# Kernel optimization log

Hardware: AMD Instinct MI355X
Metric: run time of the kernel (lower is better)

The kernel has to match this reference:

```python
import jax, jax.numpy as jnp
import numpy as np

EPS_BN = 1e-5
NEG_SLOPE = 0.2

def gat_layer(x, src, dst, N, W, a_src, a_dst, b, heads, ch, concat):
    # x: [N, Fin]; W: [Fin, heads*ch]; a_src/a_dst: [heads, ch]; b: [heads*ch] or [ch]
    xw = (x @ W).reshape(N, heads, ch)                      # [N,H,C]
    al_src = jnp.einsum('nhc,hc->nh', xw, a_src)            # [N,H]
    al_dst = jnp.einsum('nhc,hc->nh', xw, a_dst)
    e = jax.nn.leaky_relu(al_src[src] + al_dst[dst], NEG_SLOPE)  # [E,H]
    m = jax.ops.segment_max(e, dst, num_segments=N)         # segment softmax (stable)
    ee = jnp.exp(e - m[dst])
    s = jax.ops.segment_sum(ee, dst, num_segments=N)
    alpha = ee / (s[dst] + 1e-16)                            # [E,H]
    msg = xw[src] * alpha[:, :, None]                        # [E,H,C]
    out = jax.ops.segment_sum(msg, dst, num_segments=N)      # [N,H,C]
    if concat:
        return out.reshape(N, heads * ch) + b
    return out.mean(axis=1) + b

def setup_inputs():
    key = jax.random.key(0)
    ks = jax.random.split(key, 24)
    N, E, dim_in, dim_out = 20000, 320000, 256, 16
    x = jax.random.normal(ks[0], (N, dim_in), dtype=jnp.float32)
    edge_index = jax.random.randint(ks[1], (2, E), 0, N, dtype=jnp.int64)
    def glorot(k, shape):
        fan = shape[0] + shape[-1]
        return jax.random.uniform(k, shape, jnp.float32, -1.0, 1.0) * np.sqrt(6.0 / fan)
    return {
        'x': x, 'edge_index': edge_index,
        'bn_gamma': jnp.ones((dim_in,), jnp.float32),
        'bn_beta': jnp.zeros((dim_in,), jnp.float32),
        'W1': glorot(ks[2], (dim_in, 16 * 64)),
        'a1_src': glorot(ks[3], (16, 64)), 'a1_dst': glorot(ks[4], (16, 64)),
        'b1': jnp.zeros((16 * 64,), jnp.float32),
        'p1': jnp.float32(0.25),
        'W2': glorot(ks[5], (dim_in + 16 * 64, 8 * 8)),
        'a2_src': glorot(ks[6], (8, 8)), 'a2_dst': glorot(ks[7], (8, 8)),
        'b2': jnp.zeros((8 * 8,), jnp.float32),
        'p2': jnp.float32(0.25),
        'W3': glorot(ks[8], (8 * 8, 8 * dim_out)),
        'a3_src': glorot(ks[9], (8, dim_out)), 'a3_dst': glorot(ks[10], (8, dim_out)),
        'b3': jnp.zeros((dim_out,), jnp.float32),
    }

def reference(x, edge_index, bn_gamma, bn_beta, W1, a1_src, a1_dst, b1, p1,
              W2, a2_src, a2_dst, b2, p2, W3, a3_src, a3_dst, b3):
    N = x.shape[0]
    # PyG GATConv default add_self_loops=True
    loops = jnp.arange(N, dtype=edge_index.dtype)
    src = jnp.concatenate([edge_index[0], loops])
    dst = jnp.concatenate([edge_index[1], loops])
    # BatchNorm1d (training-mode batch stats)
    mu = x.mean(axis=0)
    var = x.var(axis=0)
    x_in = (x - mu) * jax.lax.rsqrt(var + EPS_BN) * bn_gamma + bn_beta
    h = gat_layer(x_in, src, dst, N, W1, a1_src, a1_dst, b1, 16, 64, True)
    h = jnp.where(h >= 0, h, p1 * h)  # PReLU
    h = gat_layer(jnp.concatenate([x_in, h], axis=1), src, dst, N, W2, a2_src, a2_dst, b2, 8, 8, True)
    h = jnp.where(h >= 0, h, p2 * h)
    h = gat_layer(h, src, dst, N, W3, a3_src, a3_dst, b3, 8, b3.shape[0], False)
    return jax.nn.log_softmax(h, axis=1)
```

## Files before the change

### kernel.cpp

```cpp
#include <hip/hip_runtime.h>
#include <math.h>

typedef unsigned int u32;
typedef unsigned short u16;
typedef u32 u32x4 __attribute__((ext_vector_type(4)));
typedef float f32x4 __attribute__((ext_vector_type(4)));

__device__ __forceinline__ u16 f2bf(float f) {
  u32 u = __builtin_bit_cast(u32, f);
  return (u16)((u + 0x7FFFu + ((u >> 16) & 1u)) >> 16);
}
__device__ __forceinline__ float bf2f(u32 lo16) {
  return __builtin_bit_cast(float, lo16 << 16);
}
__device__ __forceinline__ void mfma16(f32x4& c, const u32x4& a, const u32x4& b) {
  asm volatile("v_mfma_f32_16x16x32_bf16 %0, %1, %2, %0" : "+v"(c) : "v"(a), "v"(b));
}
__device__ __forceinline__ float lrelu(float e) { return fmaxf(e, 0.2f * e); }

__global__ void bn_stats_kernel(const float* __restrict__ x, float* __restrict__ musum,
                                float* __restrict__ sqsum, int N, int F) {
  int t = threadIdx.x;
  float s = 0.f, s2 = 0.f;
  for (int r = blockIdx.x; r < N; r += gridDim.x) {
    float v = x[(size_t)r * F + t];
    s += v;
    s2 += v * v;
  }
  atomicAdd(&musum[t], s);
  atomicAdd(&sqsum[t], s2);
}

__global__ void bn_finalize_kernel(const float* __restrict__ musum, const float* __restrict__ sqsum,
                                   const float* __restrict__ gamma, const float* __restrict__ beta,
                                   float* __restrict__ scale, float* __restrict__ shift, int N) {
  int t = threadIdx.x;
  float m = musum[t] / (float)N;
  float v = sqsum[t] / (float)N - m * m;
  float sc = gamma[t] * rsqrtf(v + 1e-5f);
  scale[t] = sc;
  shift[t] = beta[t] - m * sc;
}

__global__ void bn_apply_bf16_kernel(const float* __restrict__ x, const float* __restrict__ scale,
                                     const float* __restrict__ shift, u16* __restrict__ xin,
                                     int total, int Fmask) {
  int i = blockIdx.x * blockDim.x + threadIdx.x;
  if (i < total) {
    int c = i & Fmask;
    xin[i] = f2bf(x[i] * scale[c] + shift[c]);
  }
}

__global__ void csr_count_kernel(const int* __restrict__ ei, int E, int N, int* __restrict__ cnt) {
  int e = blockIdx.x * blockDim.x + threadIdx.x;
  int ET = E + N;
  if (e < ET) {
    int d = (e < E) ? ei[E + e] : (e - E);
    atomicAdd(&cnt[d], 1);
  }
}

__global__ __launch_bounds__(1024) void csr_scan_kernel(const int* __restrict__ cnt,
                                                        int* __restrict__ row_ptr,
                                                        int* __restrict__ cursor, int N) {
  __shared__ int part[1024];
  int t = threadIdx.x;
  int chunk = (N + 1023) / 1024;
  int lo = t * chunk;
  int hi = min(lo + chunk, N);
  int s = 0;
  for (int i = lo; i < hi; i++) s += cnt[i];
  part[t] = s;
  __syncthreads();
  for (int off = 1; off < 1024; off <<= 1) {
    int v = (t >= off) ? part[t - off] : 0;
    __syncthreads();
    part[t] += v;
    __syncthreads();
  }
  int run = (t == 0) ? 0 : part[t - 1];
  for (int i = lo; i < hi; i++) {
    row_ptr[i] = run;
    cursor[i] = run;
    run += cnt[i];
  }
  if (t == 1023) row_ptr[N] = part[1023];
}

__global__ void csr_fill_kernel(const int* __restrict__ ei, int E, int N,
                                int* __restrict__ cursor, int* __restrict__ csr_src) {
  int e = blockIdx.x * blockDim.x + threadIdx.x;
  int ET = E + N;
  if (e < ET) {
    int s, d;
    if (e < E) { s = ei[e]; d = ei[E + e]; }
    else       { s = e - E; d = s; }
    int pos = atomicAdd(&cursor[d], 1);
    csr_src[pos] = s;
  }
}

__global__ __launch_bounds__(1024) void perm_build_kernel(const int* __restrict__ row_ptr,
                                                          int* __restrict__ perm, int N) {
  __shared__ int bins[256];
  __shared__ int base[256];
  int t = threadIdx.x;
  if (t < 256) bins[t] = 0;
  __syncthreads();
  for (int i = t; i < N; i += 1024) {
    int d = min(row_ptr[i + 1] - row_ptr[i], 255);
    atomicAdd(&bins[d], 1);
  }
  __syncthreads();
  for (int off = 1; off < 256; off <<= 1) {
    int u = (t < 256 && t >= off) ? bins[t - off] : 0;
    __syncthreads();
    if (t < 256) bins[t] += u;
    __syncthreads();
  }
  if (t < 256) base[t] = (t == 0) ? 0 : bins[t - 1];
  __syncthreads();
  if (t < 256) bins[t] = base[t];
  __syncthreads();
  for (int i = t; i < N; i += 1024) {
    int d = min(row_ptr[i + 1] - row_ptr[i], 255);
    int pos = atomicAdd(&bins[d], 1);
    perm[pos] = i;
  }
}

__global__ void wt_build_all(const float* __restrict__ W1, const float* __restrict__ W2,
                             const float* __restrict__ W3, u16* __restrict__ Wt1,
                             u16* __restrict__ Wt2, u16* __restrict__ Wt3) {
  const int S1 = 1024 * 256, S2 = 64 * 1280, S3 = 128 * 64;
  const int P1 = 96 * 256, P2 = 32 * 1280, P3 = 32 * 64;
  int idx = blockIdx.x * blockDim.x + threadIdx.x;
  if (idx < S1) {
    int n = idx / 256, k = idx % 256;
    Wt1[idx] = f2bf(W1[(size_t)k * 1024 + n]);
  } else if (idx < S1 + S2) {
    int i = idx - S1;
    int n = i / 1280, k = i % 1280;
    Wt2[i] = f2bf(W2[(size_t)k * 64 + n]);
  } else if (idx < S1 + S2 + S3) {
    int i = idx - S1 - S2;
    int n = i / 64, k = i % 64;
    Wt3[i] = f2bf(W3[(size_t)k * 128 + n]);
  } else if (idx < S1 + S2 + S3 + P1) {
    Wt1[S1 + (idx - S1 - S2 - S3)] = 0;
  } else if (idx < S1 + S2 + S3 + P1 + P2) {
    Wt2[S2 + (idx - S1 - S2 - S3 - P1)] = 0;
  } else if (idx < S1 + S2 + S3 + P1 + P2 + P3) {
    Wt3[S3 + (idx - S1 - S2 - S3 - P1 - P2)] = 0;
  }
}

__global__ void alfold_build(const float* __restrict__ W1, const float* __restrict__ a1s,
                             const float* __restrict__ a1d, const float* __restrict__ W2,
                             const float* __restrict__ a2s, const float* __restrict__ a2d,
                             const float* __restrict__ W3, const float* __restrict__ a3s,
                             const float* __restrict__ a3d, u16* __restrict__ Wt1,
                             u16* __restrict__ Wt2, u16* __restrict__ Wt3) {
  const int T1 = 32 * 256, T2 = 16 * 1280, T3 = 16 * 64;
  int idx = blockIdx.x * blockDim.x + threadIdx.x;
  if (idx < T1) {
    int jj = idx / 256, k = idx % 256, h = jj >> 1;
    const float* av = (jj & 1) ? a1d : a1s;
    float s = 0.f;
    for (int c = 0; c < 64; c++) s += W1[(size_t)k * 1024 + h * 64 + c] * av[h * 64 + c];
    Wt1[(size_t)(1024 + jj) * 256 + k] = f2bf(s);
  } else if (idx < T1 + T2) {
    int i = idx - T1;
    int jj = i / 1280, k = i % 1280, h = jj >> 1;
    const float* av = (jj & 1) ? a2d : a2s;
    float s = 0.f;
    for (int c = 0; c < 8; c++) s += W2[(size_t)k * 64 + h * 8 + c] * av[h * 8 + c];
    Wt2[(size_t)(64 + jj) * 1280 + k] = f2bf(s);
  } else if (idx < T1 + T2 + T3) {
    int i = idx - T1 - T2;
    int jj = i / 64, k = i % 64, h = jj >> 1;
    const float* av = (jj & 1) ? a3d : a3s;
    float s = 0.f;
    for (int c = 0; c < 16; c++) s += W3[(size_t)k * 128 + h * 16 + c] * av[h * 16 + c];
    Wt3[(size_t)(128 + jj) * 64 + k] = f2bf(s);
  }
}

template <int BM, int BN, int FM, int FN>
__global__ __launch_bounds__(256) void mfma_gemm_al(
    const u16* __restrict__ A1, const u16* __restrict__ A2, int K1, int K,
    const u16* __restrict__ Wt, u16* __restrict__ Ch, int NcH,
    float* __restrict__ als, float* __restrict__ ald, int ALN, int ALP, int M) {
  constexpr int BK = 32;
  constexpr int ACH = (BM * BK) / 8;
  constexpr int BCH = (BN * BK) / 8;
  static_assert(BM == 2 * FM * 16 && BN == 2 * FN * 16, "wave grid 2x2");
  __shared__ u16 As[2][BM * BK];
  __shared__ u16 Bs[2][BN * BK];
  int t = threadIdx.x;
  int m0 = blockIdx.x * BM, n0 = blockIdx.y * BN;
  int r = t & 15;
  int g = (t >> 4) & 3;
  int wid = t >> 6;
  int wm0 = (wid >> 1) * (FM * 16);
  int wn0 = (wid & 1) * (FN * 16);
  int K8 = K >> 3;
  int K2 = K - K1;

  auto stage = [&](int buf, int k0) {
    const u16* Aseg;
    int sA, kl;
    if (k0 < K1) { Aseg = A1; sA = K1; kl = k0; }
    else         { Aseg = A2; sA = K2; kl = k0 - K1; }
#pragma unroll
    for (int i = 0; i < (ACH + 255) / 256; i++) {
      int c = i * 256 + t;
      if (ACH % 256 == 0 || c < ACH) {
        int m = c >> 2, kb = c & 3;
        __builtin_amdgcn_global_load_lds(
            (const __attribute__((address_space(1))) void*)(Aseg + (size_t)(m0 + m) * sA + kl + kb * 8),
            (__attribute__((address_space(3))) void*)(&As[buf][c * 8]), 16, 0, 0);
      }
    }
#pragma unroll
    for (int i = 0; i < (BCH + 255) / 256; i++) {
      int c = i * 256 + t;
      if (BCH % 256 == 0 || c < BCH) {
        int nn = c >> 2, kb = c & 3;
        __builtin_amdgcn_global_load_lds(
            (const __attribute__((address_space(1))) void*)(Wt + ((size_t)(n0 + nn) * K8 + (k0 >> 3) + kb) * 8),
            (__attribute__((address_space(3))) void*)(&Bs[buf][c * 8]), 16, 0, 0);
      }
    }
  };

  f32x4 acc[FM][FN] = {};
  asm volatile("s_nop 7\n\ts_nop 7" :::);

  stage(0, 0);
  __syncthreads();
  int nt = K / BK;
  for (int ts = 0; ts < nt; ts++) {
    if (ts + 1 < nt) stage((ts + 1) & 1, (ts + 1) * BK);
    int cur = ts & 1;
    u32x4 af[FM], bfr[FN];
#pragma unroll
    for (int fi = 0; fi < FM; fi++)
      af[fi] = *(const u32x4*)(&As[cur][((wm0 + fi * 16 + r) * 4 + g) * 8]);
#pragma unroll
    for (int fj = 0; fj < FN; fj++)
      bfr[fj] = *(const u32x4*)(&Bs[cur][((wn0 + fj * 16 + r) * 4 + g) * 8]);
#pragma unroll
    for (int fi = 0; fi < FM; fi++)
#pragma unroll
      for (int fj = 0; fj < FN; fj++) mfma16(acc[fi][fj], af[fi], bfr[fj]);
    __syncthreads();
  }
  asm volatile("s_nop 7\n\ts_nop 7" :::);

#pragma unroll
  for (int fi = 0; fi < FM; fi++) {
#pragma unroll
    for (int fj = 0; fj < FN; fj++) {
#pragma unroll
      for (int v = 0; v < 4; v++) {
        int m = m0 + wm0 + fi * 16 + g * 4 + v;
        int nn = n0 + wn0 + fj * 16 + r;
        if (m < M) {
          float val = acc[fi][fj][v];
          if (nn < NcH) {
            Ch[(size_t)m * NcH + nn] = f2bf(val);
          } else {
            int j = nn - NcH;
            if (j < ALN) ((j & 1) ? ald : als)[(size_t)(j >> 1) * ALP + m] = val;
          }
        }
      }
    }
  }
}

__global__ __launch_bounds__(256) void gat_agg1_gs(
    const u16* __restrict__ xwh, const float* __restrict__ alsrc,
    const float* __restrict__ aldst, const int* __restrict__ row_ptr,
    const int* __restrict__ csr_src, const int* __restrict__ perm,
    const float* __restrict__ bias, const float* __restrict__ slope_p,
    u16* __restrict__ out, int N, int ALP, int NBH) {
  constexpr int U = 4;
  int b = blockIdx.x;
  int xcd = b & 7, seq = b >> 3;
  int phase = seq / NBH, nb = seq - phase * NBH;
  int h = xcd + (phase << 3);
  int lane = threadIdx.x & 63;
  int g = lane >> 3, l8 = lane & 7;
  int ti = nb * 32 + (threadIdx.x >> 6) * 8 + g;
  int n = perm[min(ti, N - 1)];
  const float* alh = alsrc + (size_t)h * ALP;
  float ad = aldst[(size_t)h * ALP + n];
  int start = row_ptr[n];
  int end = row_ptr[n + 1];
  int deg = (ti < N) ? end - start : 0;
  int endm1 = end - 1;

  float m = -1e30f, s = 0.f;
  float acc[8] = {};
  const u16* base = xwh + (size_t)h * 64 + (size_t)l8 * 8;

  auto fma8 = [&](const u32x4& v, float w) {
#pragma unroll
    for (int i = 0; i < 4; i++) {
      u32 u = v[i];
      acc[2 * i] = fmaf(w, bf2f(u & 0xffffu), acc[2 * i]);
      acc[2 * i + 1] = fmaf(w, bf2f(u >> 16), acc[2 * i + 1]);
    }
  };

  int c[U];
#pragma unroll
  for (int i = 0; i < U; i++) c[i] = csr_src[min(start + i, endm1)];
  int j = 0;
  for (; j + U <= deg; j += U) {
    u32x4 v[U];
    float e[U];
#pragma unroll
    for (int i = 0; i < U; i++) v[i] = *(const u32x4*)(base + (size_t)c[i] * 1024);
#pragma unroll
    for (int i = 0; i < U; i++) e[i] = lrelu(alh[c[i]] + ad);
#pragma unroll
    for (int i = 0; i < U; i++) c[i] = csr_src[min(start + j + U + i, endm1)];
    float mn = fmaxf(fmaxf(e[0], e[1]), fmaxf(e[2], e[3]));
    if (mn > m) {
      float sc = __expf(m - mn);
      s *= sc;
#pragma unroll
      for (int k = 0; k < 8; k++) acc[k] *= sc;
      m = mn;
    }
#pragma unroll
    for (int i = 0; i < U; i++) {
      float w = __expf(e[i] - m);
      s += w;
      fma8(v[i], w);
    }
  }
  for (int i = 0; j < deg; j++, i++) {
    u32x4 v = *(const u32x4*)(base + (size_t)c[i] * 1024);
    float e = lrelu(alh[c[i]] + ad);
    if (e > m) {
      float sc = __expf(m - e);
      s *= sc;
#pragma unroll
      for (int k = 0; k < 8; k++) acc[k] *= sc;
      m = e;
    }
    float w = __expf(e - m);
    s += w;
    fma8(v, w);
  }
  float rr = 1.f / (s + 1e-16f);

  if (ti < N) {
    float p = slope_p[0];
    u32 ow[4];
#pragma unroll
    for (int i = 0; i < 4; i++) {
      int cc = h * 64 + l8 * 8 + 2 * i;
      float v0 = acc[2 * i] * rr + bias[cc];
      float v1 = acc[2 * i + 1] * rr + bias[cc + 1];
      v0 = (v0 >= 0.f) ? v0 : p * v0;
      v1 = (v1 >= 0.f) ? v1 : p * v1;
      ow[i] = (u32)f2bf(v0) | ((u32)f2bf(v1) << 16);
    }
    *(u32x4*)(out + (size_t)n * 1024 + h * 64 + l8 * 8) = *(u32x4*)ow;
  }
}

__global__ __launch_bounds__(256) void gat_agg2_gs(
    const u16* __restrict__ xwh, const float* __restrict__ alsrc,
    const float* __restrict__ aldst, const int* __restrict__ row_ptr,
    const int* __restrict__ csr_src, const int* __restrict__ perm,
    const float* __restrict__ bias, const float* __restrict__ slope_p,
    u16* __restrict__ out, int N, int ALP) {
  constexpr int U = 4;
  int lane = threadIdx.x & 63;
  int g = lane >> 3, l8 = lane & 7;
  int ti = blockIdx.x * 32 + (threadIdx.x >> 6) * 8 + g;
  int n = perm[min(ti, N - 1)];
  const float* alh = alsrc + (size_t)l8 * ALP;
  float ad = aldst[(size_t)l8 * ALP + n];
  int start = row_ptr[n];
  int end = row_ptr[n + 1];
  int deg = (ti < N) ? end - start : 0;
  int endm1 = end - 1;

  float m = -1e30f, s = 0.f;
  float acc[8] = {};
  const u16* base = xwh + (size_t)l8 * 8;

  auto fma8 = [&](const u32x4& v, float w) {
#pragma unroll
    for (int i = 0; i < 4; i++) {
      u32 u = v[i];
      acc[2 * i] = fmaf(w, bf2f(u & 0xffffu), acc[2 * i]);
      acc[2 * i + 1] = fmaf(w, bf2f(u >> 16), acc[2 * i + 1]);
    }
  };

  int c[U];
#pragma unroll
  for (int i = 0; i < U; i++) c[i] = csr_src[min(start + i, endm1)];
  int j = 0;
  for (; j + U <= deg; j += U) {
    u32x4 v[U];
    float e[U];
#pragma unroll
    for (int i = 0; i < U; i++) v[i] = *(const u32x4*)(base + (size_t)c[i] * 64);
#pragma unroll
    for (int i = 0; i < U; i++) e[i] = lrelu(alh[c[i]] + ad);
#pragma unroll
    for (int i = 0; i < U; i++) c[i] = csr_src[min(start + j + U + i, endm1)];
    float mn = fmaxf(fmaxf(e[0], e[1]), fmaxf(e[2], e[3]));
    if (mn > m) {
      float sc = __expf(m - mn);
      s *= sc;
#pragma unroll
      for (int k = 0; k < 8; k++) acc[k] *= sc;
      m = mn;
    }
#pragma unroll
    for (int i = 0; i < U; i++) {
      float w = __expf(e[i] - m);
      s += w;
      fma8(v[i], w);
    }
  }
  for (int i = 0; j < deg; j++, i++) {
    u32x4 v = *(const u32x4*)(base + (size_t)c[i] * 64);
    float e = lrelu(alh[c[i]] + ad);
    if (e > m) {
      float sc = __expf(m - e);
      s *= sc;
#pragma unroll
      for (int k = 0; k < 8; k++) acc[k] *= sc;
      m = e;
    }
    float w = __expf(e - m);
    s += w;
    fma8(v, w);
  }
  float rr = 1.f / (s + 1e-16f);

  if (ti < N) {
    float p = slope_p[0];
    u32 ow[4];
#pragma unroll
    for (int i = 0; i < 4; i++) {
      int cc = l8 * 8 + 2 * i;
      float v0 = acc[2 * i] * rr + bias[cc];
      float v1 = acc[2 * i + 1] * rr + bias[cc + 1];
      v0 = (v0 >= 0.f) ? v0 : p * v0;
      v1 = (v1 >= 0.f) ? v1 : p * v1;
      ow[i] = (u32)f2bf(v0) | ((u32)f2bf(v1) << 16);
    }
    *(u32x4*)(out + (size_t)n * 64 + l8 * 8) = *(u32x4*)ow;
  }
}

__global__ __launch_bounds__(256) void gat_agg3_gs(
    const u16* __restrict__ xwh, const float* __restrict__ alsrc,
    const float* __restrict__ aldst, const int* __restrict__ row_ptr,
    const int* __restrict__ csr_src, const int* __restrict__ perm,
    const float* __restrict__ bias, float* __restrict__ out, int N, int ALP) {
  constexpr int U = 4;
  int lane = threadIdx.x & 63;
  int g = lane >> 4, l16 = lane & 15;
  int head = l16 >> 1;
  int ti = blockIdx.x * 16 + (threadIdx.x >> 6) * 4 + g;
  int n = perm[min(ti, N - 1)];
  const float* alh = alsrc + (size_t)head * ALP;
  float ad = aldst[(size_t)head * ALP + n];
  int start = row_ptr[n];
  int end = row_ptr[n + 1];
  int deg = (ti < N) ? end - start : 0;
  int endm1 = end - 1;

  float m = -1e30f, s = 0.f;
  float acc[8] = {};
  const u16* base = xwh + (size_t)l16 * 8;

  auto fma8 = [&](const u32x4& v, float w) {
#pragma unroll
    for (int i = 0; i < 4; i++) {
      u32 u = v[i];
      acc[2 * i] = fmaf(w, bf2f(u & 0xffffu), acc[2 * i]);
      acc[2 * i + 1] = fmaf(w, bf2f(u >> 16), acc[2 * i + 1]);
    }
  };

  int c[U];
#pragma unroll
  for (int i = 0; i < U; i++) c[i] = csr_src[min(start + i, endm1)];
  int j = 0;
  for (; j + U <= deg; j += U) {
    u32x4 v[U];
    float e[U];
#pragma unroll
    for (int i = 0; i < U; i++) v[i] = *(const u32x4*)(base + (size_t)c[i] * 128);
#pragma unroll
    for (int i = 0; i < U; i++) e[i] = lrelu(alh[c[i]] + ad);
#pragma unroll
    for (int i = 0; i < U; i++) c[i] = csr_src[min(start + j + U + i, endm1)];
    float mn = fmaxf(fmaxf(e[0], e[1]), fmaxf(e[2], e[3]));
    if (mn > m) {
      float sc = __expf(m - mn);
      s *= sc;
#pragma unroll
      for (int k = 0; k < 8; k++) acc[k] *= sc;
      m = mn;
    }
#pragma unroll
    for (int i = 0; i < U; i++) {
      float w = __expf(e[i] - m);
      s += w;
      fma8(v[i], w);
    }
  }
  for (int i = 0; j < deg; j++, i++) {
    u32x4 v = *(const u32x4*)(base + (size_t)c[i] * 128);
    float e = lrelu(alh[c[i]] + ad);
    if (e > m) {
      float sc = __expf(m - e);
      s *= sc;
#pragma unroll
      for (int k = 0; k < 8; k++) acc[k] *= sc;
      m = e;
    }
    float w = __expf(e - m);
    s += w;
    fma8(v, w);
  }
  float rr = 1.f / (s + 1e-16f);
#pragma unroll
  for (int k = 0; k < 8; k++) acc[k] *= rr;

#pragma unroll
  for (int st = 2; st <= 8; st <<= 1)
#pragma unroll
    for (int k = 0; k < 8; k++) acc[k] += __shfl_xor(acc[k], st);

  int half = l16 & 1;
  float v8[8];
  float mx = -1e30f;
#pragma unroll
  for (int k = 0; k < 8; k++) {
    v8[k] = acc[k] * 0.125f + bias[half * 8 + k];
    mx = fmaxf(mx, v8[k]);
  }
  mx = fmaxf(mx, __shfl_xor(mx, 1));
  float se = 0.f;
#pragma unroll
  for (int k = 0; k < 8; k++) se += __expf(v8[k] - mx);
  se += __shfl_xor(se, 1);
  float lse = mx + logf(se);
  if (ti < N && l16 < 2) {
    float4 o0 = make_float4(v8[0] - lse, v8[1] - lse, v8[2] - lse, v8[3] - lse);
    float4 o1 = make_float4(v8[4] - lse, v8[5] - lse, v8[6] - lse, v8[7] - lse);
    float* op = out + (size_t)n * 16 + half * 8;
    *(float4*)op = o0;
    *(float4*)(op + 4) = o1;
  }
}

extern "C" void kernel_launch(void* const* d_in, const int* in_sizes, int n_in,
                              void* d_out, int out_size, void* d_ws, size_t ws_size,
                              hipStream_t stream) {
  const float* x        = (const float*)d_in[0];
  const int*   ei       = (const int*)d_in[1];
  const float* bn_gamma = (const float*)d_in[2];
  const float* bn_beta  = (const float*)d_in[3];
  const float* W1       = (const float*)d_in[4];
  const float* a1s      = (const float*)d_in[5];
  const float* a1d      = (const float*)d_in[6];
  const float* b1       = (const float*)d_in[7];
  const float* p1       = (const float*)d_in[8];
  const float* W2       = (const float*)d_in[9];
  const float* a2s      = (const float*)d_in[10];
  const float* a2d      = (const float*)d_in[11];
  const float* b2       = (const float*)d_in[12];
  const float* p2       = (const float*)d_in[13];
  const float* W3       = (const float*)d_in[14];
  const float* a3s      = (const float*)d_in[15];
  const float* a3d      = (const float*)d_in[16];
  const float* b3       = (const float*)d_in[17];
  float* out = (float*)d_out;

  const int F  = in_sizes[2];
  const int N  = in_sizes[0] / F;
  const int E  = in_sizes[1] / 2;
  const int ET = E + N;
  const int MP = ((N + 127) / 128) * 128;

  size_t off = 0;
  auto alloc = [&](size_t bytes) -> char* {
    char* r = (char*)d_ws + off;
    off += (bytes + 255) & ~(size_t)255;
    return r;
  };
  float* musum   = (float*)alloc(F * 4);
  float* sqsum   = (float*)alloc(F * 4);
  float* scale   = (float*)alloc(F * 4);
  float* shift   = (float*)alloc(F * 4);
  int*   row_ptr = (int*)alloc((size_t)(N + 1) * 4);
  int*   cursor  = (int*)alloc((size_t)N * 4);
  int*   csr_src = (int*)alloc((size_t)ET * 4);
  int*   perm    = (int*)alloc((size_t)N * 4);
  float* al_s    = (float*)alloc((size_t)16 * MP * 4);
  float* al_d    = (float*)alloc((size_t)16 * MP * 4);
  u16*   Wt1     = (u16*)alloc((size_t)1152 * 256 * 2);
  u16*   Wt2     = (u16*)alloc((size_t)96 * 1280 * 2);
  u16*   Wt3     = (u16*)alloc((size_t)160 * 64 * 2);
  u16*   x_in_h  = (u16*)alloc((size_t)MP * 256 * 2);
  u16*   xw1h    = (u16*)alloc((size_t)MP * 1024 * 2);
  u16*   h1      = (u16*)alloc((size_t)MP * 1024 * 2);
  u16*   xw2h    = (u16*)alloc((size_t)MP * 64 * 2);
  u16*   h2h     = (u16*)alloc((size_t)MP * 64 * 2);
  u16*   xw3h    = (u16*)alloc((size_t)MP * 128 * 2);

  hipMemsetAsync(musum, 0, (size_t)2 * F * 4, stream);
  bn_stats_kernel<<<256, 256, 0, stream>>>(x, musum, sqsum, N, F);
  bn_finalize_kernel<<<1, F, 0, stream>>>(musum, sqsum, bn_gamma, bn_beta, scale, shift, N);
  int totalXF = N * F;
  bn_apply_bf16_kernel<<<(totalXF + 255) / 256, 256, 0, stream>>>(x, scale, shift, x_in_h,
                                                                  totalXF, F - 1);

  hipMemsetAsync(cursor, 0, (size_t)N * 4, stream);
  csr_count_kernel<<<(ET + 255) / 256, 256, 0, stream>>>(ei, E, N, cursor);
  csr_scan_kernel<<<1, 1024, 0, stream>>>(cursor, row_ptr, cursor, N);
  csr_fill_kernel<<<(ET + 255) / 256, 256, 0, stream>>>(ei, E, N, cursor, csr_src);

  perm_build_kernel<<<1, 1024, 0, stream>>>(row_ptr, perm, N);

  {
    int total = 1024 * 256 + 64 * 1280 + 128 * 64 + 96 * 256 + 32 * 1280 + 32 * 64;
    wt_build_all<<<(total + 255) / 256, 256, 0, stream>>>(W1, W2, W3, Wt1, Wt2, Wt3);
    int tot2 = 32 * 256 + 16 * 1280 + 16 * 64;
    alfold_build<<<(tot2 + 255) / 256, 256, 0, stream>>>(W1, a1s, a1d, W2, a2s, a2d, W3, a3s, a3d,
                                                         Wt1, Wt2, Wt3);
  }

  {
    dim3 grid(MP / 128, 9);
    mfma_gemm_al<128, 128, 4, 4><<<grid, 256, 0, stream>>>(
        x_in_h, x_in_h, 256, 256, Wt1, xw1h, 1024, al_s, al_d, 32, MP, N);
    int NBH = (N + 31) / 32;
    gat_agg1_gs<<<8 * NBH * 2, 256, 0, stream>>>(xw1h, al_s, al_d, row_ptr, csr_src, perm, b1, p1,
                                                 h1, N, MP, NBH);
  }

  {
    dim3 grid((N + 63) / 64, 1);
    mfma_gemm_al<64, 96, 2, 3><<<grid, 256, 0, stream>>>(
        x_in_h, h1, 256, 1280, Wt2, xw2h, 64, al_s, al_d, 16, MP, N);
    gat_agg2_gs<<<(N + 31) / 32, 256, 0, stream>>>(xw2h, al_s, al_d, row_ptr, csr_src, perm, b2,
                                                   p2, h2h, N, MP);
  }

  {
    dim3 grid((N + 63) / 64, 1);
    mfma_gemm_al<64, 160, 2, 5><<<grid, 256, 0, stream>>>(
        h2h, h2h, 64, 64, Wt3, xw3h, 128, al_s, al_d, 16, MP, N);
    gat_agg3_gs<<<(N + 15) / 16, 256, 0, stream>>>(xw3h, al_s, al_d, row_ptr, csr_src, perm, b3,
                                                   out, N, MP);
  }
}
```

Before: 316.3 us.

## Fuse setup kernels to cut launches and raise layer-1 aggregation unroll

Merges BN finalize into the BN apply kernel, merges perm building into the CSR scan, and merges the weight transpose with the attention-fold build. It also folds the cursor memset into the stats memset. Together these remove several kernel launches and a memset from the fixed per-call overhead. The layer-1 aggregation unroll goes from 4 to 6 edges per iteration, which adds register pressure in exchange for more loads in flight. The zero-padding ranges were narrowed so they no longer overwrite the alfold rows in the same launch.

```diff
diff --git a/kernel.cpp b/kernel.cpp
--- a/kernel.cpp
+++ b/kernel.cpp
@@ -31,24 +31,19 @@
   atomicAdd(&sqsum[t], s2);
 }
 
-__global__ void bn_finalize_kernel(const float* __restrict__ musum, const float* __restrict__ sqsum,
-                                   const float* __restrict__ gamma, const float* __restrict__ beta,
-                                   float* __restrict__ scale, float* __restrict__ shift, int N) {
+__global__ void bn_apply_bf16_kernel(const float* __restrict__ x, const float* __restrict__ musum,
+                                     const float* __restrict__ sqsum,
+                                     const float* __restrict__ gamma,
+                                     const float* __restrict__ beta, u16* __restrict__ xin,
+                                     int N, float invN) {
   int t = threadIdx.x;
-  float m = musum[t] / (float)N;
-  float v = sqsum[t] / (float)N - m * m;
-  float sc = gamma[t] * rsqrtf(v + 1e-5f);
-  scale[t] = sc;
-  shift[t] = beta[t] - m * sc;
-}
-
-__global__ void bn_apply_bf16_kernel(const float* __restrict__ x, const float* __restrict__ scale,
-                                     const float* __restrict__ shift, u16* __restrict__ xin,
-                                     int total, int Fmask) {
-  int i = blockIdx.x * blockDim.x + threadIdx.x;
-  if (i < total) {
-    int c = i & Fmask;
-    xin[i] = f2bf(x[i] * scale[c] + shift[c]);
+  float mu = musum[t] * invN;
+  float var = sqsum[t] * invN - mu * mu;
+  float sc = gamma[t] * rsqrtf(var + 1e-5f);
+  float sh = beta[t] - mu * sc;
+  for (int r = blockIdx.x; r < N; r += gridDim.x) {
+    size_t idx = (size_t)r * 256 + t;
+    xin[idx] = f2bf(x[idx] * sc + sh);
   }
 }
 
@@ -61,16 +56,24 @@
   }
 }
 
-__global__ __launch_bounds__(1024) void csr_scan_kernel(const int* __restrict__ cnt,
-                                                        int* __restrict__ row_ptr,
-                                                        int* __restrict__ cursor, int N) {
+__global__ __launch_bounds__(1024) void csr_scan_perm_kernel(int* __restrict__ cnt,
+                                                             int* __restrict__ row_ptr,
+                                                             int* __restrict__ perm, int N) {
   __shared__ int part[1024];
+  __shared__ int bins[256];
+  __shared__ int bs[256];
   int t = threadIdx.x;
   int chunk = (N + 1023) / 1024;
-  int lo = t * chunk;
+  int lo = min(t * chunk, N);
   int hi = min(lo + chunk, N);
+  if (t < 256) bins[t] = 0;
+  __syncthreads();
   int s = 0;
-  for (int i = lo; i < hi; i++) s += cnt[i];
+  for (int i = lo; i < hi; i++) {
+    int d = cnt[i];
+    s += d;
+    atomicAdd(&bins[min(d, 255)], 1);
+  }
   part[t] = s;
   __syncthreads();
   for (int off = 1; off < 1024; off <<= 1) {
@@ -79,11 +82,28 @@
     part[t] += v;
     __syncthreads();
   }
+  if (t < 256) bs[t] = bins[t];
+  __syncthreads();
+  for (int off = 1; off < 256; off <<= 1) {
+    int v = (t < 256 && t >= off) ? bs[t - off] : 0;
+    __syncthreads();
+    if (t < 256) bs[t] += v;
+    __syncthreads();
+  }
+  if (t < 256) bins[t] = (t == 0) ? 0 : bs[t - 1];
+  __syncthreads();
+  for (int i = lo; i < hi; i++) {
+    int d = min(cnt[i], 255);
+    int pos = atomicAdd(&bins[d], 1);
+    perm[pos] = i;
+  }
+  __syncthreads();
   int run = (t == 0) ? 0 : part[t - 1];
   for (int i = lo; i < hi; i++) {
+    int d = cnt[i];
     row_ptr[i] = run;
-    cursor[i] = run;
-    run += cnt[i];
+    cnt[i] = run;
+    run += d;
   }
   if (t == 1023) row_ptr[N] = part[1023];
 }
@@ -101,90 +121,67 @@
   }
 }
 
-__global__ __launch_bounds__(1024) void perm_build_kernel(const int* __restrict__ row_ptr,
-                                                          int* __restrict__ perm, int N) {
-  __shared__ int bins[256];
-  __shared__ int base[256];
-  int t = threadIdx.x;
-  if (t < 256) bins[t] = 0;
-  __syncthreads();
-  for (int i = t; i < N; i += 1024) {
-    int d = min(row_ptr[i + 1] - row_ptr[i], 255);
-    atomicAdd(&bins[d], 1);
-  }
-  __syncthreads();
-  for (int off = 1; off < 256; off <<= 1) {
-    int u = (t < 256 && t >= off) ? bins[t - off] : 0;
-    __syncthreads();
-    if (t < 256) bins[t] += u;
-    __syncthreads();
-  }
-  if (t < 256) base[t] = (t == 0) ? 0 : bins[t - 1];
-  __syncthreads();
-  if (t < 256) bins[t] = base[t];
-  __syncthreads();
-  for (int i = t; i < N; i += 1024) {
-    int d = min(row_ptr[i + 1] - row_ptr[i], 255);
-    int pos = atomicAdd(&bins[d], 1);
-    perm[pos] = i;
-  }
-}
-
-__global__ void wt_build_all(const float* __restrict__ W1, const float* __restrict__ W2,
-                             const float* __restrict__ W3, u16* __restrict__ Wt1,
-                             u16* __restrict__ Wt2, u16* __restrict__ Wt3) {
+__global__ void wt_alfold_build(const float* __restrict__ W1, const float* __restrict__ a1s,
+                                const float* __restrict__ a1d, const float* __restrict__ W2,
+                                const float* __restrict__ a2s, const float* __restrict__ a2d,
+                                const float* __restrict__ W3, const float* __restrict__ a3s,
+                                const float* __restrict__ a3d, u16* __restrict__ Wt1,
+                                u16* __restrict__ Wt2, u16* __restrict__ Wt3) {
   const int S1 = 1024 * 256, S2 = 64 * 1280, S3 = 128 * 64;
-  const int P1 = 96 * 256, P2 = 32 * 1280, P3 = 32 * 64;
+  const int A1 = 32 * 256, A2 = 16 * 1280, A3 = 16 * 64;
+  const int Z1 = 96 * 256, Z2 = 16 * 1280, Z3 = 16 * 64;
   int idx = blockIdx.x * blockDim.x + threadIdx.x;
-  if (idx < S1) {
-    int n = idx / 256, k = idx % 256;
-    Wt1[idx] = f2bf(W1[(size_t)k * 1024 + n]);
-  } else if (idx < S1 + S2) {
-    int i = idx - S1;
-    int n = i / 1280, k = i % 1280;
-    Wt2[i] = f2bf(W2[(size_t)k * 64 + n]);
-  } else if (idx < S1 + S2 + S3) {
-    int i = idx - S1 - S2;
-    int n = i / 64, k = i % 64;
-    Wt3[i] = f2bf(W3[(size_t)k * 128 + n]);
-  } else if (idx < S1 + S2 + S3 + P1) {
-    Wt1[S1 + (idx - S1 - S2 - S3)] = 0;
-  } else if (idx < S1 + S2 + S3 + P1 + P2) {
-    Wt2[S2 + (idx - S1 - S2 - S3 - P1)] = 0;
-  } else if (idx < S1 + S2 + S3 + P1 + P2 + P3) {
-    Wt3[S3 + (idx - S1 - S2 - S3 - P1 - P2)] = 0;
-  }
-}
-
-__global__ void alfold_build(const float* __restrict__ W1, const float* __restrict__ a1s,
-                             const float* __restrict__ a1d, const float* __restrict__ W2,
-                             const float* __restrict__ a2s, const float* __restrict__ a2d,
-                             const float* __restrict__ W3, const float* __restrict__ a3s,
-                             const float* __restrict__ a3d, u16* __restrict__ Wt1,
-                             u16* __restrict__ Wt2, u16* __restrict__ Wt3) {
-  const int T1 = 32 * 256, T2 = 16 * 1280, T3 = 16 * 64;
-  int idx = blockIdx.x * blockDim.x + threadIdx.x;
-  if (idx < T1) {
-    int jj = idx / 256, k = idx % 256, h = jj >> 1;
+  int o = idx;
+  if (o < S1) {
+    int n = o / 256, k = o % 256;
+    Wt1[o] = f2bf(W1[(size_t)k * 1024 + n]);
+    return;
+  }
+  o -= S1;
+  if (o < S2) {
+    int n = o / 1280, k = o % 1280;
+    Wt2[o] = f2bf(W2[(size_t)k * 64 + n]);
+    return;
+  }
+  o -= S2;
+  if (o < S3) {
+    int n = o / 64, k = o % 64;
+    Wt3[o] = f2bf(W3[(size_t)k * 128 + n]);
+    return;
+  }
+  o -= S3;
+  if (o < A1) {
+    int jj = o / 256, k = o % 256, h = jj >> 1;
     const float* av = (jj & 1) ? a1d : a1s;
     float s = 0.f;
     for (int c = 0; c < 64; c++) s += W1[(size_t)k * 1024 + h * 64 + c] * av[h * 64 + c];
     Wt1[(size_t)(1024 + jj) * 256 + k] = f2bf(s);
-  } else if (idx < T1 + T2) {
-    int i = idx - T1;
-    int jj = i / 1280, k = i % 1280, h = jj >> 1;
+    return;
+  }
+  o -= A1;
+  if (o < A2) {
+    int jj = o / 1280, k = o % 1280, h = jj >> 1;
     const float* av = (jj & 1) ? a2d : a2s;
     float s = 0.f;
     for (int c = 0; c < 8; c++) s += W2[(size_t)k * 64 + h * 8 + c] * av[h * 8 + c];
     Wt2[(size_t)(64 + jj) * 1280 + k] = f2bf(s);
-  } else if (idx < T1 + T2 + T3) {
-    int i = idx - T1 - T2;
-    int jj = i / 64, k = i % 64, h = jj >> 1;
+    return;
+  }
+  o -= A2;
+  if (o < A3) {
+    int jj = o / 64, k = o % 64, h = jj >> 1;
     const float* av = (jj & 1) ? a3d : a3s;
     float s = 0.f;
     for (int c = 0; c < 16; c++) s += W3[(size_t)k * 128 + h * 16 + c] * av[h * 16 + c];
     Wt3[(size_t)(128 + jj) * 64 + k] = f2bf(s);
-  }
+    return;
+  }
+  o -= A3;
+  if (o < Z1) { Wt1[1056 * 256 + o] = 0; return; }
+  o -= Z1;
+  if (o < Z2) { Wt2[80 * 1280 + o] = 0; return; }
+  o -= Z2;
+  if (o < Z3) { Wt3[144 * 64 + o] = 0; return; }
 }
 
 template <int BM, int BN, int FM, int FN>
@@ -287,7 +284,7 @@
     const int* __restrict__ csr_src, const int* __restrict__ perm,
     const float* __restrict__ bias, const float* __restrict__ slope_p,
     u16* __restrict__ out, int N, int ALP, int NBH) {
-  constexpr int U = 4;
+  constexpr int U = 6;
   int b = blockIdx.x;
   int xcd = b & 7, seq = b >> 3;
   int phase = seq / NBH, nb = seq - phase * NBH;
@@ -329,7 +326,7 @@
     for (int i = 0; i < U; i++) e[i] = lrelu(alh[c[i]] + ad);
 #pragma unroll
     for (int i = 0; i < U; i++) c[i] = csr_src[min(start + j + U + i, endm1)];
-    float mn = fmaxf(fmaxf(e[0], e[1]), fmaxf(e[2], e[3]));
+    float mn = fmaxf(fmaxf(fmaxf(e[0], e[1]), fmaxf(e[2], e[3])), fmaxf(e[4], e[5]));
     if (mn > m) {
       float sc = __expf(m - mn);
       s *= sc;
@@ -609,10 +606,8 @@
   };
   float* musum   = (float*)alloc(F * 4);
   float* sqsum   = (float*)alloc(F * 4);
-  float* scale   = (float*)alloc(F * 4);
-  float* shift   = (float*)alloc(F * 4);
+  int*   cursor  = (int*)alloc((size_t)N * 4);
   int*   row_ptr = (int*)alloc((size_t)(N + 1) * 4);
-  int*   cursor  = (int*)alloc((size_t)N * 4);
   int*   csr_src = (int*)alloc((size_t)ET * 4);
   int*   perm    = (int*)alloc((size_t)N * 4);
   float* al_s    = (float*)alloc((size_t)16 * MP * 4);
@@ -627,26 +622,22 @@
   u16*   h2h     = (u16*)alloc((size_t)MP * 64 * 2);
   u16*   xw3h    = (u16*)alloc((size_t)MP * 128 * 2);
 
-  hipMemsetAsync(musum, 0, (size_t)2 * F * 4, stream);
+  hipMemsetAsync(musum, 0, (size_t)2 * F * 4 + (size_t)N * 4, stream);
+
   bn_stats_kernel<<<256, 256, 0, stream>>>(x, musum, sqsum, N, F);
-  bn_finalize_kernel<<<1, F, 0, stream>>>(musum, sqsum, bn_gamma, bn_beta, scale, shift, N);
-  int totalXF = N * F;
-  bn_apply_bf16_kernel<<<(totalXF + 255) / 256, 256, 0, stream>>>(x, scale, shift, x_in_h,
-                                                                  totalXF, F - 1);
-
-  hipMemsetAsync(cursor, 0, (size_t)N * 4, stream);
+  bn_apply_bf16_kernel<<<1024, 256, 0, stream>>>(x, musum, sqsum, bn_gamma, bn_beta, x_in_h, N,
+                                                 1.0f / (float)N);
+
   csr_count_kernel<<<(ET + 255) / 256, 256, 0, stream>>>(ei, E, N, cursor);
-  csr_scan_kernel<<<1, 1024, 0, stream>>>(cursor, row_ptr, cursor, N);
+  csr_scan_perm_kernel<<<1, 1024, 0, stream>>>(cursor, row_ptr, perm, N);
   csr_fill_kernel<<<(ET + 255) / 256, 256, 0, stream>>>(ei, E, N, cursor, csr_src);
 
-  perm_build_kernel<<<1, 1024, 0, stream>>>(row_ptr, perm, N);
-
   {
-    int total = 1024 * 256 + 64 * 1280 + 128 * 64 + 96 * 256 + 32 * 1280 + 32 * 64;
-    wt_build_all<<<(total + 255) / 256, 256, 0, stream>>>(W1, W2, W3, Wt1, Wt2, Wt3);
-    int tot2 = 32 * 256 + 16 * 1280 + 16 * 64;
-    alfold_build<<<(tot2 + 255) / 256, 256, 0, stream>>>(W1, a1s, a1d, W2, a2s, a2d, W3, a3s, a3d,
-                                                         Wt1, Wt2, Wt3);
+    int total = 1024 * 256 + 64 * 1280 + 128 * 64
+              + 32 * 256 + 16 * 1280 + 16 * 64
+              + 96 * 256 + 16 * 1280 + 16 * 64;
+    wt_alfold_build<<<(total + 255) / 256, 256, 0, stream>>>(W1, a1s, a1d, W2, a2s, a2d, W3, a3s,
+                                                             a3d, Wt1, Wt2, Wt3);
   }
 
   {
```

New measurement: 313.1 us. Within noise of the previous version (-1.0%).
